# Optimization experiments

Hardware: AMD Instinct MI355X
Metric: run time of the kernel (lower is better)

The kernel has to match this reference:

```python
import jax, jax.numpy as jnp
import numpy as np

B, S, D = 2, 2048, 2048
NH, NG = 16, 4          # q heads, groups
KVH = NH // NG          # kv heads = 4
HD = D // NH            # head dim = 128
ROPE_THETA = 10000.0


def _rope(t, cos, sin):
    """Rotate pairs along last dim. t: [B,S,D]; cos/sin: [S, D//2]."""
    tr = t.reshape(t.shape[:-1] + (-1, 2))  # [B,S,D/2,2] complex pairs (llama layout)
    xr, xi = tr[..., 0], tr[..., 1]
    c = cos[None, :, :]
    s = sin[None, :, :]
    yr = xr * c - xi * s
    yi = xr * s + xi * c
    return jnp.stack([yr, yi], axis=-1).reshape(t.shape)


def setup_inputs() -> dict:
    key = jax.random.key(0)
    k0, k1, k2, k3, k4 = jax.random.split(key, 5)
    scale = 1.0 / np.sqrt(D)
    x = jax.random.normal(k0, (B, S, D), jnp.float32)
    Wq = jax.random.normal(k1, (D, D), jnp.float32) * scale          # torch Linear: (out,in)
    Wk = jax.random.normal(k2, (D // NG, D), jnp.float32) * scale
    Wv = jax.random.normal(k3, (D // NG, D), jnp.float32) * scale
    Wo = jax.random.normal(k4, (D, D), jnp.float32) * scale
    mask = jnp.triu(jnp.ones((S, S), bool), k=1)[None, None]          # causal: True = masked
    return {"x": x, "Wq": Wq, "Wk": Wk, "Wv": Wv, "Wo": Wo, "mask": mask}


def reference(x, Wq, Wk, Wv, Wo, mask):
    b, s, d = x.shape
    q = x @ Wq.T                                  # [B,S,D]
    k = x @ Wk.T                                  # [B,S,D/NG]
    v = x @ Wv.T
    # repeat_kv: [B,S,KVH,HD] -> repeat each kv head NG times -> [B,S,NH,HD]
    k = jnp.repeat(k.reshape(b, s, KVH, HD), NG, axis=2).reshape(b, s, d)
    v = jnp.repeat(v.reshape(b, s, KVH, HD), NG, axis=2).reshape(b, s, d)
    # RoPE with freqs precomputed over the FULL hidden dim (as in source)
    freqs = 1.0 / (ROPE_THETA ** (jnp.arange(0, d, 2, dtype=jnp.float32) / d))  # [D/2]
    ang = jnp.arange(s, dtype=jnp.float32)[:, None] * freqs[None, :]            # [S,D/2]
    cos, sin = jnp.cos(ang), jnp.sin(ang)
    q = _rope(q, cos, sin)
    k = _rope(k, cos, sin)
    # split heads: [B,NH,S,HD]
    qh = q.reshape(b, s, NH, HD).transpose(0, 2, 1, 3)
    kh = k.reshape(b, s, NH, HD).transpose(0, 2, 1, 3)
    vh = v.reshape(b, s, NH, HD).transpose(0, 2, 1, 3)
    # NOTE: source scales by sqrt(hidden_dim), not sqrt(head_dim)
    scores = jnp.einsum('bhqd,bhkd->bhqk', qh, kh) / jnp.sqrt(jnp.float32(d))
    scores = jnp.where(mask, -jnp.inf, scores)
    probs = jax.nn.softmax(scores, axis=-1)
    out = jnp.einsum('bhqk,bhkd->bhqd', probs, vh)
    out = out.transpose(0, 2, 1, 3).reshape(b, s, d)
    return out @ Wo.T  # dropout is identity in eval
```

## Files before the change

### kernel.cpp

```cpp
#include <hip/hip_runtime.h>
#include <hip/hip_bf16.h>
#include <stdint.h>

typedef unsigned short u16;
typedef u16 u16x4 __attribute__((ext_vector_type(4)));
typedef unsigned u32x4 __attribute__((ext_vector_type(4)));
typedef __bf16 bf16x8 __attribute__((ext_vector_type(8)));
typedef float f32x4 __attribute__((ext_vector_type(4)));
typedef float f32x16 __attribute__((ext_vector_type(16)));

#define DEVI __device__ __forceinline__

DEVI u16 f2b(float f) {
  __hip_bfloat16 h = __float2bfloat16(f);
  return __builtin_bit_cast(u16, h);
}

DEVI unsigned pk2(float lo, float hi) {
  return (unsigned)f2b(lo) | ((unsigned)f2b(hi) << 16);
}

DEVI f32x4 mfma16(bf16x8 a, bf16x8 b, f32x4 c) {
  return __builtin_amdgcn_mfma_f32_16x16x32_bf16(a, b, c, 0, 0, 0);
}

DEVI f32x16 mfma32(bf16x8 a, bf16x8 b, f32x16 c) {
  return __builtin_amdgcn_mfma_f32_32x32x16_bf16(a, b, c, 0, 0, 0);
}

DEVI void gld_lds16(const u16* g, u16* l) {
  __builtin_amdgcn_global_load_lds(
      (const __attribute__((address_space(1))) unsigned int*)g,
      (__attribute__((address_space(3))) unsigned int*)l, 16, 0, 0);
}

__global__ void prep(const float4* __restrict__ x, const float4* __restrict__ wq,
                     const float4* __restrict__ wk, const float4* __restrict__ wv,
                     const float4* __restrict__ wo,
                     u16x4* __restrict__ xb, u16x4* __restrict__ wqb,
                     u16x4* __restrict__ wkb, u16x4* __restrict__ wvb,
                     u16x4* __restrict__ wob, float2* __restrict__ csT) {
  long bid = blockIdx.x;
  if (bid < 8192) {
    int i = (int)bid * 256 + threadIdx.x;
    int s = i >> 10, p = i & 1023;
    float freq = exp2f((float)p * -0.012976281620653759f);
    float ang = (float)s * freq;
    float sv, cv;
    __sincosf(ang, &sv, &cv);
    csT[i] = make_float2(cv, sv);
    return;
  }
  long i = (bid - 8192) * 256 + threadIdx.x;
  const float4* src; u16x4* dst; long o;
  if (i < 2097152)      { src = x;  dst = xb;  o = i; }
  else if (i < 3145728) { src = wq; dst = wqb; o = i - 2097152; }
  else if (i < 3407872) { src = wk; dst = wkb; o = i - 3145728; }
  else if (i < 3670016) { src = wv; dst = wvb; o = i - 3407872; }
  else                  { src = wo; dst = wob; o = i - 3670016; }
  float4 v = src[o];
  u16x4 r = { f2b(v.x), f2b(v.y), f2b(v.z), f2b(v.w) };
  dst[o] = r;
}

__global__ __launch_bounds__(512)
void gemm_qkv(const u16* __restrict__ A, const u16* __restrict__ wq,
              const u16* __restrict__ wk, const u16* __restrict__ wv,
              const float2* __restrict__ csT, u16* __restrict__ Qh,
              u16* __restrict__ Kh, u16* __restrict__ Vtp) {
  __shared__ __align__(16) u16 lds[3][16384];
  const int tid = threadIdx.x;
  const int lane = tid & 63;
  const int w = tid >> 6;
  const int wr = w >> 2, wc = w & 3;
  const int x = blockIdx.x, m0 = blockIdx.y << 8, n0 = x << 8;
  const int K = 2048;

  const u16* Bw;
  int mode;
  if (x < 8)       { Bw = wq + (size_t)n0 * K;          mode = 0; }
  else if (x < 10) { Bw = wk + (size_t)(n0 - 2048) * K; mode = 1; }
  else             { Bw = wv + (size_t)(n0 - 2560) * K; mode = 2; }

  const int srow = tid >> 2;
  const int cs = (tid & 3) ^ ((srow >> 1) & 3);
  const int p = srow & 63, p4 = p >> 4, pl = p & 15;
  const int prow = (srow & ~63) | (pl << 1) | (p4 & 1) | ((p4 & 2) << 4);
  const int bsrc = (mode == 2) ? srow : prow;
  const u16* ga0 = A + (size_t)(m0 + srow) * K + (cs << 3);
  const u16* gb0 = Bw + (size_t)bsrc * K + (cs << 3);
  const size_t rstep = (size_t)128 * K;

  f32x4 acc[8][4] = {};
  const int nk = K >> 5;

#define QKV_STAGE(buf, ks)                                        \
  {                                                               \
    u16* l0 = &lds[buf][tid << 3];                                \
    const u16* ga_ = ga0 + ((size_t)(ks) << 5);                   \
    const u16* gb_ = gb0 + ((size_t)(ks) << 5);                   \
    gld_lds16(ga_, l0);                                           \
    gld_lds16(ga_ + rstep, l0 + 4096);                            \
    gld_lds16(gb_, l0 + 8192);                                    \
    gld_lds16(gb_ + rstep, l0 + 12288);                           \
  }

  QKV_STAGE(0, 0);
  QKV_STAGE(1, 1);

  const int l15 = lane & 15;
  const int lg = lane >> 4;
  const int ch8 = (lg ^ ((l15 >> 1) & 3)) << 3;
  const int arow0 = (wr << 7) + l15;
  const int brow0 = (wc << 6) + l15;

  int bufc = 0;
  for (int kt = 0; kt < nk; ++kt) {
    asm volatile("s_waitcnt vmcnt(4)" ::: "memory");
    __builtin_amdgcn_sched_barrier(0);
    __builtin_amdgcn_s_barrier();
    {
      const int ts = (kt + 2 < nk) ? kt + 2 : nk - 1;
      const int bufn = bufc ? bufc - 1 : 2;
      QKV_STAGE(bufn, ts);
    }
    const u16* la = &lds[bufc][0];
    const u16* lb = &lds[bufc][8192];
    bf16x8 af[8], bfr[4];
#pragma unroll
    for (int mi = 0; mi < 8; ++mi)
      af[mi] = *(const bf16x8*)&la[((arow0 + (mi << 4)) << 5) + ch8];
#pragma unroll
    for (int ni = 0; ni < 4; ++ni)
      bfr[ni] = *(const bf16x8*)&lb[((brow0 + (ni << 4)) << 5) + ch8];
    __builtin_amdgcn_s_setprio(1);
#pragma unroll
    for (int mi = 0; mi < 8; ++mi)
#pragma unroll
      for (int ni = 0; ni < 4; ++ni)
        acc[mi][ni] = mfma16(af[mi], bfr[ni], acc[mi][ni]);
    __builtin_amdgcn_s_setprio(0);
    bufc = (bufc == 2) ? 0 : bufc + 1;
  }
  asm volatile("s_waitcnt vmcnt(0)" ::: "memory");
#undef QKV_STAGE

  const int crow = (lane >> 4) << 2;
  if (mode == 0) {
    const float SCL = 0.022097086912079608f * 1.4426950408889634f;
    const int h = (x << 1) + (wc >> 1);
    const int hd0 = ((wc & 1) << 6) + (l15 << 1);
    const int tb = (h << 6) + ((wc & 1) << 5) + l15;
#pragma unroll
    for (int mi = 0; mi < 8; ++mi)
#pragma unroll
      for (int rr = 0; rr < 4; ++rr) {
        int row = m0 + (wr << 7) + (mi << 4) + crow + rr;
        int s = row & 2047, b = row >> 11;
        float2 cA = csT[(s << 10) + tb];
        float2 cB = csT[(s << 10) + tb + 16];
        float v0 = acc[mi][0][rr], v1 = acc[mi][1][rr];
        float v2 = acc[mi][2][rr], v3 = acc[mi][3][rr];
        unsigned lo = pk2((v0 * cA.x - v1 * cA.y) * SCL, (v0 * cA.y + v1 * cA.x) * SCL);
        unsigned hi = pk2((v2 * cB.x - v3 * cB.y) * SCL, (v2 * cB.y + v3 * cB.x) * SCL);
        u16* dst = &Qh[((size_t)(b * 16 + h) * 2048 + s) * 128 + hd0];
        *(unsigned*)dst = lo;
        *(unsigned*)(dst + 32) = hi;
      }
  } else if (mode == 1) {
    const int kvh = ((x - 8) << 1) + (wc >> 1);
    const int hd0 = ((wc & 1) << 6) + (l15 << 1);
#pragma unroll
    for (int mi = 0; mi < 8; ++mi)
#pragma unroll
      for (int rr = 0; rr < 4; ++rr) {
        int row = m0 + (wr << 7) + (mi << 4) + crow + rr;
        int s = row & 2047, b = row >> 11;
        float v0 = acc[mi][0][rr], v1 = acc[mi][1][rr];
        float v2 = acc[mi][2][rr], v3 = acc[mi][3][rr];
#pragma unroll
        for (int g = 0; g < 4; ++g) {
          int h = (kvh << 2) + g;
          int tb = (h << 6) + ((wc & 1) << 5) + l15;
          float2 cA = csT[(s << 10) + tb];
          float2 cB = csT[(s << 10) + tb + 16];
          unsigned lo = pk2(v0 * cA.x - v1 * cA.y, v0 * cA.y + v1 * cA.x);
          unsigned hi = pk2(v2 * cB.x - v3 * cB.y, v2 * cB.y + v3 * cB.x);
          u16* dst = &Kh[((size_t)(b * 16 + h) * 2048 + s) * 128 + hd0];
          *(unsigned*)dst = lo;
          *(unsigned*)(dst + 32) = hi;
        }
      }
  } else {
#pragma unroll
    for (int mi = 0; mi < 8; ++mi) {
      int sg = m0 + (wr << 7) + (mi << 4) + crow;
      int b = sg >> 11, s = sg & 2047;
#pragma unroll
      for (int ni = 0; ni < 4; ++ni) {
        int n = ((x - 10) << 8) + (wc << 6) + (ni << 4) + l15;
        u16x4 pk = { f2b(acc[mi][ni][0]), f2b(acc[mi][ni][1]),
                     f2b(acc[mi][ni][2]), f2b(acc[mi][ni][3]) };
        *(u16x4*)&Vtp[((size_t)((b << 2) + (n >> 7)) * 128 + (n & 127)) * 2048 + s] = pk;
      }
    }
  }
}

__global__ __launch_bounds__(512)
void gemm_bt(const u16* __restrict__ A, const u16* __restrict__ Bw,
             float* __restrict__ C, int M, int N, int K) {
  __shared__ __align__(16) u16 lds[3][16384];
  const int tid = threadIdx.x;
  const int lane = tid & 63;
  const int w = tid >> 6;
  const int wr = w >> 2, wc = w & 3;
  const int m0 = blockIdx.y << 8, n0 = blockIdx.x << 8;

  const int srow = tid >> 2;
  const int cs = (tid & 3) ^ ((srow >> 1) & 3);
  const u16* ga0 = A + (size_t)(m0 + srow) * K + (cs << 3);
  const u16* gb0 = Bw + (size_t)(n0 + srow) * K + (cs << 3);
  const size_t rstep = (size_t)128 * K;

  f32x4 acc[8][4] = {};
  const int nk = K >> 5;

#define BT_STAGE(buf, ks)                                         \
  {                                                               \
    u16* l0 = &lds[buf][tid << 3];                                \
    const u16* ga_ = ga0 + ((size_t)(ks) << 5);                   \
    const u16* gb_ = gb0 + ((size_t)(ks) << 5);                   \
    gld_lds16(ga_, l0);                                           \
    gld_lds16(ga_ + rstep, l0 + 4096);                            \
    gld_lds16(gb_, l0 + 8192);                                    \
    gld_lds16(gb_ + rstep, l0 + 12288);                           \
  }

  BT_STAGE(0, 0);
  BT_STAGE(1, 1);

  const int l15 = lane & 15;
  const int lg = lane >> 4;
  const int ch8 = (lg ^ ((l15 >> 1) & 3)) << 3;
  const int arow0 = (wr << 7) + l15;
  const int brow0 = (wc << 6) + l15;

  int bufc = 0;
  for (int kt = 0; kt < nk; ++kt) {
    asm volatile("s_waitcnt vmcnt(4)" ::: "memory");
    __builtin_amdgcn_sched_barrier(0);
    __builtin_amdgcn_s_barrier();
    {
      const int ts = (kt + 2 < nk) ? kt + 2 : nk - 1;
      const int bufn = bufc ? bufc - 1 : 2;
      BT_STAGE(bufn, ts);
    }
    const u16* la = &lds[bufc][0];
    const u16* lb = &lds[bufc][8192];
    bf16x8 af[8], bfr[4];
#pragma unroll
    for (int mi = 0; mi < 8; ++mi)
      af[mi] = *(const bf16x8*)&la[((arow0 + (mi << 4)) << 5) + ch8];
#pragma unroll
    for (int ni = 0; ni < 4; ++ni)
      bfr[ni] = *(const bf16x8*)&lb[((brow0 + (ni << 4)) << 5) + ch8];
    __builtin_amdgcn_s_setprio(1);
#pragma unroll
    for (int mi = 0; mi < 8; ++mi)
#pragma unroll
      for (int ni = 0; ni < 4; ++ni)
        acc[mi][ni] = mfma16(af[mi], bfr[ni], acc[mi][ni]);
    __builtin_amdgcn_s_setprio(0);
    bufc = (bufc == 2) ? 0 : bufc + 1;
  }
  asm volatile("s_waitcnt vmcnt(0)" ::: "memory");
#undef BT_STAGE

  const int crow = (lane >> 4) << 2;
#pragma unroll
  for (int mi = 0; mi < 8; ++mi) {
    int row = m0 + (wr << 7) + (mi << 4) + crow;
#pragma unroll
    for (int ni = 0; ni < 4; ++ni) {
      int col = n0 + (wc << 6) + (ni << 4) + l15;
#pragma unroll
      for (int rr = 0; rr < 4; ++rr)
        C[(size_t)(row + rr) * N + col] = acc[mi][ni][rr];
    }
  }
}

__global__ __launch_bounds__(256, 2)
void attn_kernel(const u16* __restrict__ Qh, const u16* __restrict__ Kh,
                 const u16* __restrict__ Vt, u16* __restrict__ attnO) {
  __shared__ __align__(16) u16 lds[3][8192];
  const int tid = threadIdx.x, lane = tid & 63, w = tid >> 6;
  const int bid = blockIdx.x;
  const int x = bid & 7, j = bid >> 3;
  const int half = j >> 5, jj = j & 31;
  const int bh = (x << 2) + (jj >> 4) + (half << 1);
  const int r = jj & 15;
  const int qt = half ? r : 15 - r;
  const int h = bh & 15, b = bh >> 4;

  const int qi = lane & 31, hi = lane >> 5;
  const int q0 = (qt << 7) + (w << 5);
  const int qabs = q0 + qi;

  const u16* Qp = Qh + (size_t)(b * 16 + h) * 262144;
  const u16* Kp = Kh + (size_t)(b * 16 + h) * 262144;
  const u16* Vp = Vt + (size_t)((b << 2) + (h >> 2)) * 262144;

  bf16x8 qf[8];
#pragma unroll
  for (int kc = 0; kc < 8; ++kc)
    qf[kc] = *(const bf16x8*)&Qp[(size_t)qabs * 128 + kc * 16 + hi * 8];

  const int kRow = tid >> 4;
  const int kCl = ((tid & 15) ^ (kRow & 7)) << 3;
  const int vRow = tid >> 2;
  const int vCl = ((tid & 3) ^ ((tid >> 3) & 3)) << 3;
  const int ldsoff = tid << 3;

  f32x16 ot[4] = {};
  float mrow = -1e30f, lsum = 0.f;
  const int nt = (qt << 2) + 4;
  const int nt_w = (qt << 2) + w + 1;
  const int swq = qi & 7, swv = (qi >> 1) & 3;

#pragma unroll
  for (int pt = 0; pt < 2; ++pt) {
    u16* bb = (u16*)lds[pt];
    gld_lds16(Kp + (size_t)((pt << 5) + kRow) * 128 + kCl, bb + ldsoff);
    gld_lds16(Kp + (size_t)((pt << 5) + kRow + 16) * 128 + kCl, bb + ldsoff + 2048);
    gld_lds16(Vp + (size_t)vRow * 2048 + (pt << 5) + vCl, bb + 4096 + ldsoff);
    gld_lds16(Vp + (size_t)(vRow + 64) * 2048 + (pt << 5) + vCl, bb + 4096 + ldsoff + 2048);
  }

  int bufc = 0;
  for (int t = 0; t < nt; ++t) {
    asm volatile("s_waitcnt vmcnt(4)" ::: "memory");
    __builtin_amdgcn_sched_barrier(0);
    __builtin_amdgcn_s_barrier();
    {
      const int ts = (t + 2 < nt) ? t + 2 : nt - 1;
      const int bufn = bufc ? bufc - 1 : 2;
      u16* bb = (u16*)lds[bufn];
      gld_lds16(Kp + (size_t)((ts << 5) + kRow) * 128 + kCl, bb + ldsoff);
      gld_lds16(Kp + (size_t)((ts << 5) + kRow + 16) * 128 + kCl, bb + ldsoff + 2048);
      gld_lds16(Vp + (size_t)vRow * 2048 + (ts << 5) + vCl, bb + 4096 + ldsoff);
      gld_lds16(Vp + (size_t)(vRow + 64) * 2048 + (ts << 5) + vCl, bb + 4096 + ldsoff + 2048);
    }
    if (t < nt_w) {
      const u16* kb_ = &lds[bufc][0];
      const u16* vb_ = &lds[bufc][4096];
      f32x16 st = {};
      __builtin_amdgcn_s_setprio(1);
#pragma unroll
      for (int kc = 0; kc < 8; ++kc) {
        bf16x8 kf = *(const bf16x8*)&kb_[(qi << 7) + ((((kc << 1) + hi) ^ swq) << 3)];
        st = mfma32(kf, qf[kc], st);
      }
      __builtin_amdgcn_s_setprio(0);

      if (t == nt_w - 1) {
        const int kb0 = t << 5;
#pragma unroll
        for (int reg = 0; reg < 16; ++reg) {
          int kk = kb0 + (reg & 3) + ((reg >> 2) << 3) + (hi << 2);
          if (kk > qabs) st[reg] = -1e30f;
        }
      }

      float tmax = st[0];
#pragma unroll
      for (int reg = 1; reg < 16; ++reg) tmax = fmaxf(tmax, st[reg]);
      tmax = fmaxf(tmax, __shfl_xor(tmax, 32));

      if (__any(tmax - mrow > 11.5f)) {
        float nm = fmaxf(mrow, tmax);
        float al = __builtin_amdgcn_exp2f(mrow - nm);
        mrow = nm;
        lsum *= al;
#pragma unroll
        for (int db = 0; db < 4; ++db)
#pragma unroll
          for (int reg = 0; reg < 16; ++reg) ot[db][reg] *= al;
      }

      float psum = 0.f;
#pragma unroll
      for (int reg = 0; reg < 16; ++reg) {
        st[reg] = __builtin_amdgcn_exp2f(st[reg] - mrow);
        psum += st[reg];
      }
      psum += __shfl_xor(psum, 32);
      lsum += psum;

      bf16x8 pfrag[2];
#pragma unroll
      for (int bbp = 0; bbp < 2; ++bbp) {
        unsigned x0 = pk2(st[8 * bbp + 0], st[8 * bbp + 1]);
        unsigned x1 = pk2(st[8 * bbp + 2], st[8 * bbp + 3]);
        unsigned y0 = pk2(st[8 * bbp + 4], st[8 * bbp + 5]);
        unsigned y1 = pk2(st[8 * bbp + 6], st[8 * bbp + 7]);
        asm("v_permlane32_swap_b32 %0, %1" : "+v"(x0), "+v"(y0));
        asm("v_permlane32_swap_b32 %0, %1" : "+v"(x1), "+v"(y1));
        u32x4 uw = { x0, x1, y0, y1 };
        pfrag[bbp] = __builtin_bit_cast(bf16x8, uw);
      }

      __builtin_amdgcn_s_setprio(1);
#pragma unroll
      for (int db = 0; db < 4; ++db) {
        const u16* vr = &vb_[((db << 5) + qi) << 5];
#pragma unroll
        for (int ks = 0; ks < 2; ++ks) {
          bf16x8 vf = *(const bf16x8*)&vr[((((ks << 1) + hi)) ^ swv) << 3];
          ot[db] = mfma32(vf, pfrag[ks], ot[db]);
        }
      }
      __builtin_amdgcn_s_setprio(0);
    }
    bufc = (bufc == 2) ? 0 : bufc + 1;
  }

  float inv = 1.f / lsum;
  u16* rowp = attnO + (size_t)(b * 2048 + qabs) * 2048 + h * 128 + (hi << 2);
#pragma unroll
  for (int db = 0; db < 4; ++db)
#pragma unroll
    for (int mg = 0; mg < 4; ++mg) {
      u16x4 pkv = { f2b(ot[db][4 * mg + 0] * inv), f2b(ot[db][4 * mg + 1] * inv),
                    f2b(ot[db][4 * mg + 2] * inv), f2b(ot[db][4 * mg + 3] * inv) };
      *(u16x4*)&rowp[(db << 5) + (mg << 3)] = pkv;
    }
}

extern "C" void kernel_launch(void* const* d_in, const int* in_sizes, int n_in,
                              void* d_out, int out_size, void* d_ws, size_t ws_size,
                              hipStream_t stream) {
  const float* x  = (const float*)d_in[0];
  const float* Wq = (const float*)d_in[1];
  const float* Wk = (const float*)d_in[2];
  const float* Wv = (const float*)d_in[3];
  const float* Wo = (const float*)d_in[4];
  float* out = (float*)d_out;
  char* ws = (char*)d_ws;

  u16*    xb   = (u16*)(ws + 0);
  u16*    wqb  = (u16*)(ws + 16777216);
  u16*    wkb  = (u16*)(ws + 25165824);
  u16*    wvb  = (u16*)(ws + 27262976);
  u16*    wob  = (u16*)(ws + 29360128);
  float2* csT  = (float2*)(ws + 37748736);
  u16*    Qhp  = (u16*)(ws + 54525952);
  u16*    Khp  = (u16*)(ws + 71303168);
  u16*    Vtp  = (u16*)(ws + 88080384);
  u16*    attnb= (u16*)(ws + 92274688);

  prep<<<26624, 256, 0, stream>>>((const float4*)x, (const float4*)Wq,
                                  (const float4*)Wk, (const float4*)Wv,
                                  (const float4*)Wo, (u16x4*)xb, (u16x4*)wqb,
                                  (u16x4*)wkb, (u16x4*)wvb, (u16x4*)wob, csT);
  gemm_qkv<<<dim3(12, 16), 512, 0, stream>>>(xb, wqb, wkb, wvb, csT, Qhp, Khp, Vtp);
  attn_kernel<<<512, 256, 0, stream>>>(Qhp, Khp, Vtp, attnb);
  gemm_bt<<<dim3(8, 16), 512, 0, stream>>>(attnb, wob, out, 4096, 2048, 2048);
}
```

Baseline: 216.8 us.

## Restructure QKV and output GEMMs to double-buffered 64-wide K tiles

Both GEMM kernels move from a triple-buffered 32-wide K step to a double-buffered 64-wide K step. They use a new per-warp row-chunk load pattern with an XOR swizzle over 8 chunks, and load fragments into registers before a barrier so the next stage can overwrite the same buffer. The output GEMM also halves its M tile to 128, doubling the grid to 256 blocks to fill more CUs. The aim is to halve barrier and loop overhead per K and improve occupancy. The cost is an extra barrier per iteration and a shallower prefetch, which may expose more global latency.

```diff
diff --git a/kernel.cpp b/kernel.cpp
--- a/kernel.cpp
+++ b/kernel.cpp
@@ -32,6 +32,11 @@
   __builtin_amdgcn_global_load_lds(
       (const __attribute__((address_space(1))) unsigned int*)g,
       (__attribute__((address_space(3))) unsigned int*)l, 16, 0, 0);
+}
+
+DEVI int prow_of(int r) {
+  int p = r & 63, p4 = p >> 4, pl = p & 15;
+  return (r & ~63) | (pl << 1) | (p4 & 1) | ((p4 & 2) << 4);
 }
 
 __global__ void prep(const float4* __restrict__ x, const float4* __restrict__ wq,
@@ -68,11 +73,11 @@
               const u16* __restrict__ wk, const u16* __restrict__ wv,
               const float2* __restrict__ csT, u16* __restrict__ Qh,
               u16* __restrict__ Kh, u16* __restrict__ Vtp) {
-  __shared__ __align__(16) u16 lds[3][16384];
+  __shared__ __align__(16) u16 lds[2][32768];
   const int tid = threadIdx.x;
   const int lane = tid & 63;
-  const int w = tid >> 6;
-  const int wr = w >> 2, wc = w & 3;
+  const int w8 = tid >> 6;
+  const int wr = w8 >> 2, wc = w8 & 3;
   const int x = blockIdx.x, m0 = blockIdx.y << 8, n0 = x << 8;
   const int K = 2048;
 
@@ -82,65 +87,76 @@
   else if (x < 10) { Bw = wk + (size_t)(n0 - 2048) * K; mode = 1; }
   else             { Bw = wv + (size_t)(n0 - 2560) * K; mode = 2; }
 
-  const int srow = tid >> 2;
-  const int cs = (tid & 3) ^ ((srow >> 1) & 3);
-  const int p = srow & 63, p4 = p >> 4, pl = p & 15;
-  const int prow = (srow & ~63) | (pl << 1) | (p4 & 1) | ((p4 & 2) << 4);
-  const int bsrc = (mode == 2) ? srow : prow;
-  const u16* ga0 = A + (size_t)(m0 + srow) * K + (cs << 3);
-  const u16* gb0 = Bw + (size_t)bsrc * K + (cs << 3);
-  const size_t rstep = (size_t)128 * K;
+  const int ln8 = lane >> 3;
+  const int gch = ((lane & 7) ^ ln8) << 3;
+  const int dstoff = lane << 3;
 
   f32x4 acc[8][4] = {};
-  const int nk = K >> 5;
-
-#define QKV_STAGE(buf, ks)                                        \
-  {                                                               \
-    u16* l0 = &lds[buf][tid << 3];                                \
-    const u16* ga_ = ga0 + ((size_t)(ks) << 5);                   \
-    const u16* gb_ = gb0 + ((size_t)(ks) << 5);                   \
-    gld_lds16(ga_, l0);                                           \
-    gld_lds16(ga_ + rstep, l0 + 4096);                            \
-    gld_lds16(gb_, l0 + 8192);                                    \
-    gld_lds16(gb_ + rstep, l0 + 12288);                           \
-  }
-
-  QKV_STAGE(0, 0);
-  QKV_STAGE(1, 1);
+  const int nk = 32;
+
+#define QKV_STAGE(bufp, ks)                                               \
+  {                                                                       \
+    const int c0_ = ((ks) << 6) + gch;                                    \
+    _Pragma("unroll")                                                     \
+    for (int l = 0; l < 4; ++l) {                                         \
+      int Lr = (((w8 << 2) + l) << 3) + ln8;                              \
+      gld_lds16(A + (size_t)(m0 + Lr) * K + c0_,                          \
+                (bufp) + (((w8 << 2) + l) << 9) + dstoff);                \
+      int br = (mode == 2) ? Lr : prow_of(Lr);                            \
+      gld_lds16(Bw + (size_t)br * K + c0_,                                \
+                (bufp) + 16384 + (((w8 << 2) + l) << 9) + dstoff);        \
+    }                                                                     \
+  }
+
+  QKV_STAGE(lds[0], 0);
+  QKV_STAGE(lds[1], 1);
 
   const int l15 = lane & 15;
   const int lg = lane >> 4;
-  const int ch8 = (lg ^ ((l15 >> 1) & 3)) << 3;
-  const int arow0 = (wr << 7) + l15;
-  const int brow0 = (wc << 6) + l15;
-
-  int bufc = 0;
-  for (int kt = 0; kt < nk; ++kt) {
-    asm volatile("s_waitcnt vmcnt(4)" ::: "memory");
+  const int sw0 = (lg ^ (l15 & 7)) << 3;
+  const int sw1 = ((4 + lg) ^ (l15 & 7)) << 3;
+  const int arowb = (wr << 7) + l15;
+  const int browb = (wc << 6) + l15;
+
+  for (int t = 0; t < nk; ++t) {
+    asm volatile("s_waitcnt vmcnt(8)" ::: "memory");
+    __builtin_amdgcn_sched_barrier(0);
+    __builtin_amdgcn_s_barrier();
+    const u16* la = lds[t & 1];
+    const u16* lb = la + 16384;
+    bf16x8 af0[8], af1[8], bf0[4], bf1[4];
+#pragma unroll
+    for (int mi = 0; mi < 8; ++mi) {
+      const int ro = (arowb + (mi << 4)) << 6;
+      af0[mi] = *(const bf16x8*)&la[ro + sw0];
+      af1[mi] = *(const bf16x8*)&la[ro + sw1];
+    }
+#pragma unroll
+    for (int ni = 0; ni < 4; ++ni) {
+      const int ro = (browb + (ni << 4)) << 6;
+      bf0[ni] = *(const bf16x8*)&lb[ro + sw0];
+      bf1[ni] = *(const bf16x8*)&lb[ro + sw1];
+    }
+    asm volatile("s_waitcnt lgkmcnt(0)" ::: "memory");
     __builtin_amdgcn_sched_barrier(0);
     __builtin_amdgcn_s_barrier();
     {
-      const int ts = (kt + 2 < nk) ? kt + 2 : nk - 1;
-      const int bufn = bufc ? bufc - 1 : 2;
-      QKV_STAGE(bufn, ts);
-    }
-    const u16* la = &lds[bufc][0];
-    const u16* lb = &lds[bufc][8192];
-    bf16x8 af[8], bfr[4];
+      const int ts = (t + 2 < nk) ? t + 2 : nk - 1;
+      u16* bp = lds[t & 1];
+      QKV_STAGE(bp, ts);
+    }
+    __builtin_amdgcn_s_setprio(1);
 #pragma unroll
     for (int mi = 0; mi < 8; ++mi)
-      af[mi] = *(const bf16x8*)&la[((arow0 + (mi << 4)) << 5) + ch8];
-#pragma unroll
-    for (int ni = 0; ni < 4; ++ni)
-      bfr[ni] = *(const bf16x8*)&lb[((brow0 + (ni << 4)) << 5) + ch8];
-    __builtin_amdgcn_s_setprio(1);
+#pragma unroll
+      for (int ni = 0; ni < 4; ++ni)
+        acc[mi][ni] = mfma16(af0[mi], bf0[ni], acc[mi][ni]);
 #pragma unroll
     for (int mi = 0; mi < 8; ++mi)
 #pragma unroll
       for (int ni = 0; ni < 4; ++ni)
-        acc[mi][ni] = mfma16(af[mi], bfr[ni], acc[mi][ni]);
+        acc[mi][ni] = mfma16(af1[mi], bf1[ni], acc[mi][ni]);
     __builtin_amdgcn_s_setprio(0);
-    bufc = (bufc == 2) ? 0 : bufc + 1;
   }
   asm volatile("s_waitcnt vmcnt(0)" ::: "memory");
 #undef QKV_STAGE
@@ -210,77 +226,94 @@
 __global__ __launch_bounds__(512)
 void gemm_bt(const u16* __restrict__ A, const u16* __restrict__ Bw,
              float* __restrict__ C, int M, int N, int K) {
-  __shared__ __align__(16) u16 lds[3][16384];
+  __shared__ __align__(16) u16 lds[2][24576];
   const int tid = threadIdx.x;
   const int lane = tid & 63;
-  const int w = tid >> 6;
-  const int wr = w >> 2, wc = w & 3;
-  const int m0 = blockIdx.y << 8, n0 = blockIdx.x << 8;
-
-  const int srow = tid >> 2;
-  const int cs = (tid & 3) ^ ((srow >> 1) & 3);
-  const u16* ga0 = A + (size_t)(m0 + srow) * K + (cs << 3);
-  const u16* gb0 = Bw + (size_t)(n0 + srow) * K + (cs << 3);
-  const size_t rstep = (size_t)128 * K;
-
-  f32x4 acc[8][4] = {};
-  const int nk = K >> 5;
-
-#define BT_STAGE(buf, ks)                                         \
-  {                                                               \
-    u16* l0 = &lds[buf][tid << 3];                                \
-    const u16* ga_ = ga0 + ((size_t)(ks) << 5);                   \
-    const u16* gb_ = gb0 + ((size_t)(ks) << 5);                   \
-    gld_lds16(ga_, l0);                                           \
-    gld_lds16(ga_ + rstep, l0 + 4096);                            \
-    gld_lds16(gb_, l0 + 8192);                                    \
-    gld_lds16(gb_ + rstep, l0 + 12288);                           \
-  }
-
-  BT_STAGE(0, 0);
-  BT_STAGE(1, 1);
+  const int w8 = tid >> 6;
+  const int wr = w8 >> 2, wc = w8 & 3;
+  const int m0 = blockIdx.y << 7, n0 = blockIdx.x << 8;
+
+  const int ln8 = lane >> 3;
+  const int gch = ((lane & 7) ^ ln8) << 3;
+  const int dstoff = lane << 3;
+
+  f32x4 acc[4][4] = {};
+  const int nk = K >> 6;
+
+#define BT_STAGE(bufp, ks)                                                \
+  {                                                                       \
+    const int c0_ = ((ks) << 6) + gch;                                    \
+    _Pragma("unroll")                                                     \
+    for (int l = 0; l < 2; ++l) {                                         \
+      int Lr = (((w8 << 1) + l) << 3) + ln8;                              \
+      gld_lds16(A + (size_t)(m0 + Lr) * K + c0_,                          \
+                (bufp) + (((w8 << 1) + l) << 9) + dstoff);                \
+    }                                                                     \
+    _Pragma("unroll")                                                     \
+    for (int l = 0; l < 4; ++l) {                                         \
+      int Lr = (((w8 << 2) + l) << 3) + ln8;                              \
+      gld_lds16(Bw + (size_t)(n0 + Lr) * K + c0_,                         \
+                (bufp) + 8192 + (((w8 << 2) + l) << 9) + dstoff);         \
+    }                                                                     \
+  }
+
+  BT_STAGE(lds[0], 0);
+  BT_STAGE(lds[1], 1);
 
   const int l15 = lane & 15;
   const int lg = lane >> 4;
-  const int ch8 = (lg ^ ((l15 >> 1) & 3)) << 3;
-  const int arow0 = (wr << 7) + l15;
-  const int brow0 = (wc << 6) + l15;
-
-  int bufc = 0;
-  for (int kt = 0; kt < nk; ++kt) {
-    asm volatile("s_waitcnt vmcnt(4)" ::: "memory");
+  const int sw0 = (lg ^ (l15 & 7)) << 3;
+  const int sw1 = ((4 + lg) ^ (l15 & 7)) << 3;
+  const int arowb = (wr << 6) + l15;
+  const int browb = (wc << 6) + l15;
+
+  for (int t = 0; t < nk; ++t) {
+    asm volatile("s_waitcnt vmcnt(6)" ::: "memory");
+    __builtin_amdgcn_sched_barrier(0);
+    __builtin_amdgcn_s_barrier();
+    const u16* la = lds[t & 1];
+    const u16* lb = la + 8192;
+    bf16x8 af0[4], af1[4], bf0[4], bf1[4];
+#pragma unroll
+    for (int mi = 0; mi < 4; ++mi) {
+      const int ro = (arowb + (mi << 4)) << 6;
+      af0[mi] = *(const bf16x8*)&la[ro + sw0];
+      af1[mi] = *(const bf16x8*)&la[ro + sw1];
+    }
+#pragma unroll
+    for (int ni = 0; ni < 4; ++ni) {
+      const int ro = (browb + (ni << 4)) << 6;
+      bf0[ni] = *(const bf16x8*)&lb[ro + sw0];
+      bf1[ni] = *(const bf16x8*)&lb[ro + sw1];
+    }
+    asm volatile("s_waitcnt lgkmcnt(0)" ::: "memory");
     __builtin_amdgcn_sched_barrier(0);
     __builtin_amdgcn_s_barrier();
     {
-      const int ts = (kt + 2 < nk) ? kt + 2 : nk - 1;
-      const int bufn = bufc ? bufc - 1 : 2;
-      BT_STAGE(bufn, ts);
-    }
-    const u16* la = &lds[bufc][0];
-    const u16* lb = &lds[bufc][8192];
-    bf16x8 af[8], bfr[4];
-#pragma unroll
-    for (int mi = 0; mi < 8; ++mi)
-      af[mi] = *(const bf16x8*)&la[((arow0 + (mi << 4)) << 5) + ch8];
-#pragma unroll
-    for (int ni = 0; ni < 4; ++ni)
-      bfr[ni] = *(const bf16x8*)&lb[((brow0 + (ni << 4)) << 5) + ch8];
+      const int ts = (t + 2 < nk) ? t + 2 : nk - 1;
+      u16* bp = lds[t & 1];
+      BT_STAGE(bp, ts);
+    }
     __builtin_amdgcn_s_setprio(1);
 #pragma unroll
-    for (int mi = 0; mi < 8; ++mi)
+    for (int mi = 0; mi < 4; ++mi)
 #pragma unroll
       for (int ni = 0; ni < 4; ++ni)
-        acc[mi][ni] = mfma16(af[mi], bfr[ni], acc[mi][ni]);
+        acc[mi][ni] = mfma16(af0[mi], bf0[ni], acc[mi][ni]);
+#pragma unroll
+    for (int mi = 0; mi < 4; ++mi)
+#pragma unroll
+      for (int ni = 0; ni < 4; ++ni)
+        acc[mi][ni] = mfma16(af1[mi], bf1[ni], acc[mi][ni]);
     __builtin_amdgcn_s_setprio(0);
-    bufc = (bufc == 2) ? 0 : bufc + 1;
   }
   asm volatile("s_waitcnt vmcnt(0)" ::: "memory");
 #undef BT_STAGE
 
   const int crow = (lane >> 4) << 2;
 #pragma unroll
-  for (int mi = 0; mi < 8; ++mi) {
-    int row = m0 + (wr << 7) + (mi << 4) + crow;
+  for (int mi = 0; mi < 4; ++mi) {
+    int row = m0 + (wr << 6) + (mi << 4) + crow;
 #pragma unroll
     for (int ni = 0; ni < 4; ++ni) {
       int col = n0 + (wc << 6) + (ni << 4) + l15;
@@ -466,5 +499,5 @@
                                   (u16x4*)wkb, (u16x4*)wvb, (u16x4*)wob, csT);
   gemm_qkv<<<dim3(12, 16), 512, 0, stream>>>(xb, wqb, wkb, wvb, csT, Qhp, Khp, Vtp);
   attn_kernel<<<512, 256, 0, stream>>>(Qhp, Khp, Vtp, attnb);
-  gemm_bt<<<dim3(8, 16), 512, 0, stream>>>(attnb, wob, out, 4096, 2048, 2048);
-}
+  gemm_bt<<<dim3(8, 32), 512, 0, stream>>>(attnb, wob, out, 4096, 2048, 2048);
+}
```

After: 217.6 us. No clear change (+0.3%).

## Shrink output GEMM tile to 128x128 with double buffering and more blocks

Applied to the files above, without the earlier changes.

Reworks the final output-projection GEMM from 256x256 tiles on 512 threads with a 3-stage asynchronous pipeline to 128x128 tiles on 256 threads with 2-stage double buffering and a full __syncthreads each iteration. The grid grows from 128 to 512 blocks so the MI355X's many CUs are better filled, which addresses the under-occupancy of a 128-block launch. The cost is less data reuse per tile, more global traffic, and a less aggressive prefetch with no explicit vmcnt wait scheduling or priority hints.

```diff
diff --git a/kernel.cpp b/kernel.cpp
--- a/kernel.cpp
+++ b/kernel.cpp
@@ -207,80 +207,75 @@
   }
 }
 
-__global__ __launch_bounds__(512)
+__global__ __launch_bounds__(256)
 void gemm_bt(const u16* __restrict__ A, const u16* __restrict__ Bw,
              float* __restrict__ C, int M, int N, int K) {
-  __shared__ __align__(16) u16 lds[3][16384];
+  __shared__ __align__(16) u16 lds[2][2][4096];
   const int tid = threadIdx.x;
   const int lane = tid & 63;
   const int w = tid >> 6;
-  const int wr = w >> 2, wc = w & 3;
-  const int m0 = blockIdx.y << 8, n0 = blockIdx.x << 8;
+  const int wr = w >> 1, wc = w & 1;
+  const int m0 = blockIdx.y << 7, n0 = blockIdx.x << 7;
 
   const int srow = tid >> 2;
   const int cs = (tid & 3) ^ ((srow >> 1) & 3);
   const u16* ga0 = A + (size_t)(m0 + srow) * K + (cs << 3);
   const u16* gb0 = Bw + (size_t)(n0 + srow) * K + (cs << 3);
-  const size_t rstep = (size_t)128 * K;
-
-  f32x4 acc[8][4] = {};
+  const size_t rstep = (size_t)64 * K;
+
+  f32x4 acc[4][4] = {};
   const int nk = K >> 5;
-
-#define BT_STAGE(buf, ks)                                         \
-  {                                                               \
-    u16* l0 = &lds[buf][tid << 3];                                \
-    const u16* ga_ = ga0 + ((size_t)(ks) << 5);                   \
-    const u16* gb_ = gb0 + ((size_t)(ks) << 5);                   \
-    gld_lds16(ga_, l0);                                           \
-    gld_lds16(ga_ + rstep, l0 + 4096);                            \
-    gld_lds16(gb_, l0 + 8192);                                    \
-    gld_lds16(gb_ + rstep, l0 + 12288);                           \
-  }
-
-  BT_STAGE(0, 0);
-  BT_STAGE(1, 1);
+  int cur = 0;
+
+  {
+    u16* la = &lds[0][0][tid << 3];
+    u16* lb = &lds[0][1][tid << 3];
+    gld_lds16(ga0, la);
+    gld_lds16(ga0 + rstep, la + 2048);
+    gld_lds16(gb0, lb);
+    gld_lds16(gb0 + rstep, lb + 2048);
+  }
+  __syncthreads();
 
   const int l15 = lane & 15;
   const int lg = lane >> 4;
   const int ch8 = (lg ^ ((l15 >> 1) & 3)) << 3;
-  const int arow0 = (wr << 7) + l15;
-  const int brow0 = (wc << 6) + l15;
-
-  int bufc = 0;
+  const int abase = (((wr << 6) + l15) << 5) + ch8;
+  const int bbase = (((wc << 6) + l15) << 5) + ch8;
+
   for (int kt = 0; kt < nk; ++kt) {
-    asm volatile("s_waitcnt vmcnt(4)" ::: "memory");
-    __builtin_amdgcn_sched_barrier(0);
-    __builtin_amdgcn_s_barrier();
-    {
-      const int ts = (kt + 2 < nk) ? kt + 2 : nk - 1;
-      const int bufn = bufc ? bufc - 1 : 2;
-      BT_STAGE(bufn, ts);
-    }
-    const u16* la = &lds[bufc][0];
-    const u16* lb = &lds[bufc][8192];
-    bf16x8 af[8], bfr[4];
-#pragma unroll
-    for (int mi = 0; mi < 8; ++mi)
-      af[mi] = *(const bf16x8*)&la[((arow0 + (mi << 4)) << 5) + ch8];
+    if (kt + 1 < nk) {
+      const u16* ga = ga0 + ((size_t)(kt + 1) << 5);
+      const u16* gb = gb0 + ((size_t)(kt + 1) << 5);
+      u16* la = &lds[cur ^ 1][0][tid << 3];
+      u16* lb = &lds[cur ^ 1][1][tid << 3];
+      gld_lds16(ga, la);
+      gld_lds16(ga + rstep, la + 2048);
+      gld_lds16(gb, lb);
+      gld_lds16(gb + rstep, lb + 2048);
+    }
+    const u16* la = &lds[cur][0][0];
+    const u16* lb = &lds[cur][1][0];
+    bf16x8 af[4], bfr[4];
+#pragma unroll
+    for (int mi = 0; mi < 4; ++mi)
+      af[mi] = *(const bf16x8*)&la[abase + (mi << 9)];
 #pragma unroll
     for (int ni = 0; ni < 4; ++ni)
-      bfr[ni] = *(const bf16x8*)&lb[((brow0 + (ni << 4)) << 5) + ch8];
-    __builtin_amdgcn_s_setprio(1);
-#pragma unroll
-    for (int mi = 0; mi < 8; ++mi)
+      bfr[ni] = *(const bf16x8*)&lb[bbase + (ni << 9)];
+#pragma unroll
+    for (int mi = 0; mi < 4; ++mi)
 #pragma unroll
       for (int ni = 0; ni < 4; ++ni)
         acc[mi][ni] = mfma16(af[mi], bfr[ni], acc[mi][ni]);
-    __builtin_amdgcn_s_setprio(0);
-    bufc = (bufc == 2) ? 0 : bufc + 1;
-  }
-  asm volatile("s_waitcnt vmcnt(0)" ::: "memory");
-#undef BT_STAGE
+    __syncthreads();
+    cur ^= 1;
+  }
 
   const int crow = (lane >> 4) << 2;
 #pragma unroll
-  for (int mi = 0; mi < 8; ++mi) {
-    int row = m0 + (wr << 7) + (mi << 4) + crow;
+  for (int mi = 0; mi < 4; ++mi) {
+    int row = m0 + (wr << 6) + (mi << 4) + crow;
 #pragma unroll
     for (int ni = 0; ni < 4; ++ni) {
       int col = n0 + (wc << 6) + (ni << 4) + l15;
@@ -466,5 +461,5 @@
                                   (u16x4*)wkb, (u16x4*)wvb, (u16x4*)wob, csT);
   gemm_qkv<<<dim3(12, 16), 512, 0, stream>>>(xb, wqb, wkb, wvb, csT, Qhp, Khp, Vtp);
   attn_kernel<<<512, 256, 0, stream>>>(Qhp, Khp, Vtp, attnb);
-  gemm_bt<<<dim3(8, 16), 512, 0, stream>>>(attnb, wob, out, 4096, 2048, 2048);
-}
+  gemm_bt<<<dim3(16, 32), 256, 0, stream>>>(attnb, wob, out, 4096, 2048, 2048);
+}
```

New measurement: 204.9 us (median of 2 runs). 1.06x faster.
